# Kernel tuning notes

Hardware: AMD Instinct MI355X
Metric: run time of the kernel (lower is better)

Reference implementation:

```python
import jax, jax.numpy as jnp
import numpy as np

B, N, F, H, D, V = 1024, 64, 512, 512, 64, 16
NT = 6  # n_transform_params
SPLITS = [V * NT, NT, 1, V, V]
NOUT = sum(SPLITS)  # 135


def _make_transform(p):
    # p: [..., 6] -> similarity transform matrix [..., 3, 3], nonlinear=True
    sx, sy, theta, shear, tx, ty = [p[..., i] for i in range(6)]
    scale = jax.nn.sigmoid(sx) + 1e-2
    tx = jnp.tanh(tx * 5.0)
    ty = jnp.tanh(ty * 5.0)
    theta = theta * (2.0 * np.pi)
    c, s = jnp.cos(theta), jnp.sin(theta)
    zeros = jnp.zeros_like(scale)
    ones = jnp.ones_like(scale)
    row0 = jnp.stack([scale * c, -scale * s, tx], -1)
    row1 = jnp.stack([scale * s, scale * c, ty], -1)
    row2 = jnp.stack([zeros, zeros, ones], -1)
    return jnp.stack([row0, row1, row2], -2)


def setup_inputs() -> dict:
    key = jax.random.key(0)
    ks = jax.random.split(key, 12)
    feature = jax.random.normal(ks[0], (B, N, F), jnp.float32)
    # per-capsule feature MLP: F -> H -> D (with bias, ReLU between)
    mlp_w1 = jax.random.normal(ks[1], (N, F, H), jnp.float32) / np.sqrt(F)
    mlp_b1 = jnp.zeros((N, H), jnp.float32)
    mlp_w2 = jax.random.normal(ks[2], (N, H, D), jnp.float32) / np.sqrt(H)
    mlp_b2 = jnp.zeros((N, D), jnp.float32)
    # per-capsule caps MLP (bias=False): (D+1) -> H -> NOUT
    caps_w1 = jax.random.normal(ks[3], (N, D + 1, H), jnp.float32) / np.sqrt(D + 1)
    caps_w2 = jax.random.normal(ks[4], (N, H, NOUT), jnp.float32) / np.sqrt(H)
    # learned biases for outputs 1..4 and the static cpr
    bias_cvr = jnp.zeros((1, N, 1, NT), jnp.float32)
    bias_pl_caps = jnp.zeros((1, N, 1), jnp.float32)
    bias_pl_vote = jnp.zeros((1, N, V), jnp.float32)
    bias_scale = jnp.zeros((1, N, V), jnp.float32)
    cpr_static = jnp.zeros((1, N, V, NT), jnp.float32)
    return dict(feature=feature, mlp_w1=mlp_w1, mlp_b1=mlp_b1, mlp_w2=mlp_w2,
                mlp_b2=mlp_b2, caps_w1=caps_w1, caps_w2=caps_w2,
                bias_cvr=bias_cvr, bias_pl_caps=bias_pl_caps,
                bias_pl_vote=bias_pl_vote, bias_scale=bias_scale,
                cpr_static=cpr_static)


def reference(feature, mlp_w1, mlp_b1, mlp_w2, mlp_b2, caps_w1, caps_w2,
              bias_cvr, bias_pl_caps, bias_pl_vote, bias_scale, cpr_static):
    batch_size = feature.shape[0]
    # grouped per-capsule MLP over the capsule axis (replaces the python loop)
    h = jax.nn.relu(jnp.einsum('bnf,nfh->bnh', feature, mlp_w1) + mlp_b1[None])
    raw_caps_param = jnp.einsum('bnh,nhd->bnd', h, mlp_w2) + mlp_b2[None]  # [B,N,D]
    # dropout rate 0 -> caps_exist = ones
    caps_exist = jnp.ones((batch_size, N, 1), raw_caps_param.dtype)
    caps_param = jnp.concatenate([raw_caps_param, caps_exist], -1)  # [B,N,D+1]
    h2 = jax.nn.relu(jnp.einsum('bnd,ndh->bnh', caps_param, caps_w1))
    all_param = jnp.einsum('bnh,nho->bno', h2, caps_w2)  # [B,N,NOUT]
    offs = np.cumsum([0] + SPLITS)
    cpr_dynamic = all_param[..., offs[0]:offs[1]].reshape(batch_size, N, V, NT)
    cvr6 = all_param[..., offs[1]:offs[2]].reshape(batch_size, N, 1, NT)
    pl_caps = all_param[..., offs[2]:offs[3]].reshape(batch_size, N, 1)
    pl_vote = all_param[..., offs[3]:offs[4]].reshape(batch_size, N, V)
    scale6 = all_param[..., offs[4]:offs[5]].reshape(batch_size, N, V)
    cpr_dynamic_reg_loss = 0.5 * jnp.sum(cpr_dynamic ** 2) / batch_size
    cpr = _make_transform(cpr_dynamic + cpr_static)           # [B,N,V,3,3]
    cvr = _make_transform(cvr6 + bias_cvr)                     # [B,N,1,3,3]
    vote = jnp.matmul(cvr, cpr)                                # broadcast over V
    presence_logit_per_caps = pl_caps + bias_pl_caps
    presence_logit_per_vote = pl_vote + bias_pl_vote
    presence_per_vote = (jax.nn.sigmoid(presence_logit_per_caps)
                         * jax.nn.sigmoid(presence_logit_per_vote))
    # learn_vote_scale=True
    scale_per_vote = jax.nn.softplus(scale6 + bias_scale + 0.5) + 0.01
    return (vote, scale_per_vote, presence_per_vote,
            presence_logit_per_caps, presence_logit_per_vote,
            cpr_dynamic_reg_loss, raw_caps_param)
```

## Files before the change

kernel.cpp:

```cpp
#include <hip/hip_runtime.h>
#include <math.h>


#define BB    1024
#define NN    64
#define FF    512
#define HH    512
#define DD    64
#define VV    16
#define NTT   6
#define NOUTT 135

#define TBM     64
#define THREADS 512
#define NBLK    1024

typedef _Float16 f16;
typedef _Float16 f16x8 __attribute__((ext_vector_type(8)));
typedef float f32x4 __attribute__((ext_vector_type(4)));

#define MFMA16(a, b, c) __builtin_amdgcn_mfma_f32_16x16x32_f16((a), (b), (c), 0, 0, 0)
#define NTS(v, p)  __builtin_nontemporal_store((v), (p))

#define SZ_VOTE  ((size_t)BB*NN*VV*9)
#define OFF_VOTE  ((size_t)0)
#define OFF_SCALE (SZ_VOTE)
#define OFF_PRES  (OFF_SCALE + (size_t)BB*NN*VV)
#define OFF_PLC   (OFF_PRES  + (size_t)BB*NN*VV)
#define OFF_PLV   (OFF_PLC   + (size_t)BB*NN)
#define OFF_LOSS  (OFF_PLV   + (size_t)BB*NN*VV)
#define OFF_RAW   (OFF_LOSS  + 1)

#define WS_LOSSP 0
#define WS_W1H   ((size_t)8192)
#define WS_W2H   (WS_W1H  + 33554432)
#define WS_CW1H  (WS_W2H  + 4194304)
#define WS_CW2H  (WS_CW1H + 4194304)
#define WS_NEED  (WS_CW2H + 9437184)

__device__ __forceinline__ float sigmoidf_(float x) { return 1.f / (1.f + expf(-x)); }
__device__ __forceinline__ float softplusf_(float x) { return (x > 20.f) ? x : log1pf(expf(x)); }

__device__ __forceinline__ void make_tr(const float* p, float* M) {
  float scale = sigmoidf_(p[0]) + 1e-2f;
  float tx = tanhf(p[4] * 5.f);
  float ty = tanhf(p[5] * 5.f);
  float th = p[2] * 6.28318530717958647692f;
  float c = cosf(th), s = sinf(th);
  M[0] = scale * c; M[1] = -scale * s; M[2] = tx;
  M[3] = scale * s; M[4] =  scale * c; M[5] = ty;
  M[6] = 0.f;       M[7] = 0.f;        M[8] = 1.f;
}

__global__ void conv_fragB(const float* __restrict__ src, f16* __restrict__ dst,
                           int capStride, int Nsz, int Kc, int Nf) {
  const int tid = blockIdx.x * 256 + threadIdx.x;
  const int total = 64 * Kc * Nf * 64;
  if (tid >= total) return;
  const int c = tid & 15, g = (tid >> 4) & 3;
  int q = tid >> 6;
  const int nf = q % Nf; q /= Nf;
  const int kc = q % Kc; const int n = q / Kc;
  const int col = nf * 16 + c;
  const float* s = src + (size_t)n * capStride + (size_t)(kc * 32 + g * 8) * Nsz + col;
  f16x8 v;
  #pragma unroll
  for (int j = 0; j < 8; ++j) {
    float x = (col < Nsz) ? s[(size_t)j * Nsz] : 0.f;
    v[j] = (f16)x;
  }
  *(f16x8*)(dst + (size_t)tid * 8) = v;
}

__global__ __launch_bounds__(THREADS, 4)
void caps_mfma(const float* __restrict__ feature,
               const float* __restrict__ mlp_b1,
               const float* __restrict__ mlp_b2,
               const float* __restrict__ caps_w1,
               const f16*  __restrict__ w1h,
               const f16*  __restrict__ w2h,
               const f16*  __restrict__ cw1h,
               const f16*  __restrict__ cw2h,
               const float* __restrict__ bias_cvr,
               const float* __restrict__ bias_pl_caps,
               const float* __restrict__ bias_pl_vote,
               const float* __restrict__ bias_scale,
               const float* __restrict__ cpr_static,
               float* __restrict__ out,
               float* __restrict__ lossp)
{
  __shared__ __align__(16) f16 R0h[32768];
  __shared__ __align__(16) f16 Rraw[4096];
  __shared__ float red[8];

  const int t   = threadIdx.x;
  const int w   = t >> 6;
  const int ln  = t & 63;
  const int g   = ln >> 4;
  const int c16 = ln & 15;

  const int bid = blockIdx.x;
  const int xcd = bid & 7;
  const int j_  = bid >> 3;
  const int n   = (xcd << 3) + (j_ >> 4);
  const int b0  = (j_ & 15) * TBM;

  for (int rr = w; rr < 64; rr += 8) {
    const int mt = rr >> 4, kb = (rr & 15) * 4;
    const int koct = kb + g;
    const int brow = b0 + mt * 16 + c16;
    const float* fp = feature + ((size_t)brow * NN + n) * FF + koct * 8;
    const f32x4 f0 = __builtin_nontemporal_load((const f32x4*)fp);
    const f32x4 f1 = __builtin_nontemporal_load((const f32x4*)(fp + 4));
    f16x8 v;
    v[0]=(f16)f0.x; v[1]=(f16)f0.y; v[2]=(f16)f0.z; v[3]=(f16)f0.w;
    v[4]=(f16)f1.x; v[5]=(f16)f1.y; v[6]=(f16)f1.z; v[7]=(f16)f1.w;
    *(f16x8*)(R0h + mt * 8192 + koct * 128 + c16 * 8) = v;
  }
  __syncthreads();

  f32x4 acc[4][4];
  #pragma unroll
  for (int mt = 0; mt < 4; ++mt)
    #pragma unroll
    for (int nf = 0; nf < 4; ++nf) acc[mt][nf] = (f32x4)0.f;

  {
    const f16* wp = w1h + (size_t)n * 16 * 16384 + (size_t)(w * 4) * 512 + (size_t)ln * 8;
    f16x8 bA[4], bB[4];
    #pragma unroll
    for (int nf = 0; nf < 4; ++nf) bA[nf] = *(const f16x8*)(wp + (size_t)nf * 512);
    #pragma unroll
    for (int kc = 0; kc < 16; kc += 2) {
      #pragma unroll
      for (int nf = 0; nf < 4; ++nf)
        bB[nf] = *(const f16x8*)(wp + (size_t)(kc + 1) * 16384 + (size_t)nf * 512);
      f16x8 af[4];
      #pragma unroll
      for (int mt = 0; mt < 4; ++mt)
        af[mt] = *(const f16x8*)(R0h + mt * 8192 + (kc * 4 + g) * 128 + c16 * 8);
      #pragma unroll
      for (int nf = 0; nf < 4; ++nf)
        #pragma unroll
        for (int mt = 0; mt < 4; ++mt)
          acc[mt][nf] = MFMA16(af[mt], bA[nf], acc[mt][nf]);
      if (kc + 2 < 16) {
        #pragma unroll
        for (int nf = 0; nf < 4; ++nf)
          bA[nf] = *(const f16x8*)(wp + (size_t)(kc + 2) * 16384 + (size_t)nf * 512);
      }
      #pragma unroll
      for (int mt = 0; mt < 4; ++mt)
        af[mt] = *(const f16x8*)(R0h + mt * 8192 + ((kc + 1) * 4 + g) * 128 + c16 * 8);
      #pragma unroll
      for (int nf = 0; nf < 4; ++nf)
        #pragma unroll
        for (int mt = 0; mt < 4; ++mt)
          acc[mt][nf] = MFMA16(af[mt], bB[nf], acc[mt][nf]);
    }
  }
  __syncthreads();

  {
    const float* b1n = mlp_b1 + (size_t)n * HH;
    #pragma unroll
    for (int nf = 0; nf < 4; ++nf) {
      const int hcol = w * 64 + nf * 16 + c16;
      const float bb = b1n[hcol];
      const int koct = hcol >> 3, jj = hcol & 7;
      #pragma unroll
      for (int mt = 0; mt < 4; ++mt)
        #pragma unroll
        for (int r = 0; r < 4; ++r)
          R0h[mt * 8192 + koct * 128 + (g * 4 + r) * 8 + jj] =
              (f16)fmaxf(acc[mt][nf][r] + bb, 0.f);
    }
  }
  __syncthreads();

  {
    const int dnf = w & 3, mh = w >> 2;
    f32x4 accB0 = (f32x4)0.f, accB1 = (f32x4)0.f;
    const f16* w2p = w2h + (size_t)n * 16 * 2048 + (size_t)dnf * 512 + (size_t)ln * 8;
    f16x8 bw[16];
    #pragma unroll
    for (int kc = 0; kc < 16; ++kc) bw[kc] = *(const f16x8*)(w2p + (size_t)kc * 2048);
    #pragma unroll
    for (int kc = 0; kc < 16; ++kc) {
      const f16x8 af0 = *(const f16x8*)(R0h + (2 * mh)     * 8192 + (kc * 4 + g) * 128 + c16 * 8);
      const f16x8 af1 = *(const f16x8*)(R0h + (2 * mh + 1) * 8192 + (kc * 4 + g) * 128 + c16 * 8);
      accB0 = MFMA16(af0, bw[kc], accB0);
      accB1 = MFMA16(af1, bw[kc], accB1);
    }
    const int d = dnf * 16 + c16;
    const float bb2 = mlp_b2[(size_t)n * DD + d];
    const int koct = d >> 3, jj = d & 7;
    #pragma unroll
    for (int i = 0; i < 2; ++i) {
      const int mt = 2 * mh + i;
      const f32x4 a = i ? accB1 : accB0;
      #pragma unroll
      for (int r = 0; r < 4; ++r) {
        const int m = mt * 16 + g * 4 + r;
        const float v = a[r] + bb2;
        NTS(v, &out[OFF_RAW + (((size_t)(b0 + m)) * NN + n) * DD + d]);
        Rraw[mt * 1024 + koct * 128 + (g * 4 + r) * 8 + jj] = (f16)v;
      }
    }
  }
  __syncthreads();

  #pragma unroll
  for (int mt = 0; mt < 4; ++mt)
    #pragma unroll
    for (int nf = 0; nf < 4; ++nf) acc[mt][nf] = (f32x4)0.f;
  {
    const f16* cw1p = cw1h + (size_t)n * 2 * 16384 + (size_t)(w * 4) * 512 + (size_t)ln * 8;
    f16x8 bc0[4], bc1[4];
    #pragma unroll
    for (int nf = 0; nf < 4; ++nf) bc0[nf] = *(const f16x8*)(cw1p + (size_t)nf * 512);
    #pragma unroll
    for (int nf = 0; nf < 4; ++nf) bc1[nf] = *(const f16x8*)(cw1p + 16384 + (size_t)nf * 512);
    #pragma unroll
    for (int kc = 0; kc < 2; ++kc) {
      f16x8 af[4];
      #pragma unroll
      for (int mt = 0; mt < 4; ++mt)
        af[mt] = *(const f16x8*)(Rraw + mt * 1024 + (kc * 4 + g) * 128 + c16 * 8);
      #pragma unroll
      for (int nf = 0; nf < 4; ++nf)
        #pragma unroll
        for (int mt = 0; mt < 4; ++mt)
          acc[mt][nf] = MFMA16(af[mt], kc ? bc1[nf] : bc0[nf], acc[mt][nf]);
    }
    const float* cl = caps_w1 + ((size_t)n * 65 + 64) * HH;
    #pragma unroll
    for (int nf = 0; nf < 4; ++nf) {
      const int hcol = w * 64 + nf * 16 + c16;
      const float ev = cl[hcol];
      const int koct = hcol >> 3, jj = hcol & 7;
      #pragma unroll
      for (int mt = 0; mt < 4; ++mt)
        #pragma unroll
        for (int r = 0; r < 4; ++r)
          R0h[mt * 8192 + koct * 128 + (g * 4 + r) * 8 + jj] =
              (f16)fmaxf(acc[mt][nf][r] + ev, 0.f);
    }
  }
  __syncthreads();

  f32x4 accD[4];
  f32x4 accD8[4];
  #pragma unroll
  for (int mt = 0; mt < 4; ++mt) { accD[mt] = (f32x4)0.f; accD8[mt] = (f32x4)0.f; }
  {
    const f16* cw2p = cw2h + (size_t)n * 16 * 4608 + (size_t)ln * 8;
    const bool w0 = (w == 0);
    f16x8 dA, dB, dA8, dB8;
    dA = *(const f16x8*)(cw2p + (size_t)w * 512);
    if (w0) dA8 = *(const f16x8*)(cw2p + (size_t)8 * 512);
    #pragma unroll
    for (int kc = 0; kc < 16; kc += 2) {
      dB = *(const f16x8*)(cw2p + (size_t)(kc + 1) * 4608 + (size_t)w * 512);
      if (w0) dB8 = *(const f16x8*)(cw2p + (size_t)(kc + 1) * 4608 + (size_t)8 * 512);
      f16x8 af[4];
      #pragma unroll
      for (int mt = 0; mt < 4; ++mt)
        af[mt] = *(const f16x8*)(R0h + mt * 8192 + (kc * 4 + g) * 128 + c16 * 8);
      #pragma unroll
      for (int mt = 0; mt < 4; ++mt) accD[mt] = MFMA16(af[mt], dA, accD[mt]);
      if (w0) {
        #pragma unroll
        for (int mt = 0; mt < 4; ++mt) accD8[mt] = MFMA16(af[mt], dA8, accD8[mt]);
      }
      if (kc + 2 < 16) {
        dA = *(const f16x8*)(cw2p + (size_t)(kc + 2) * 4608 + (size_t)w * 512);
        if (w0) dA8 = *(const f16x8*)(cw2p + (size_t)(kc + 2) * 4608 + (size_t)8 * 512);
      }
      #pragma unroll
      for (int mt = 0; mt < 4; ++mt)
        af[mt] = *(const f16x8*)(R0h + mt * 8192 + ((kc + 1) * 4 + g) * 128 + c16 * 8);
      #pragma unroll
      for (int mt = 0; mt < 4; ++mt) accD[mt] = MFMA16(af[mt], dB, accD[mt]);
      if (w0) {
        #pragma unroll
        for (int mt = 0; mt < 4; ++mt) accD8[mt] = MFMA16(af[mt], dB8, accD8[mt]);
      }
    }
  }
  __syncthreads();

  float* apf = (float*)R0h;
  {
    const int col = w * 16 + c16;
    #pragma unroll
    for (int mt = 0; mt < 4; ++mt)
      #pragma unroll
      for (int r = 0; r < 4; ++r)
        apf[(size_t)(mt * 16 + g * 4 + r) * 145 + col] = accD[mt][r];
    if (w == 0) {
      const int col8 = 128 + c16;
      if (col8 < NOUTT) {
        #pragma unroll
        for (int mt = 0; mt < 4; ++mt)
          #pragma unroll
          for (int r = 0; r < 4; ++r)
            apf[(size_t)(mt * 16 + g * 4 + r) * 145 + col8] = accD8[mt][r];
      }
    }
  }
  __syncthreads();

  {
    const int mrow = t >> 3, seg = t & 7;
    const float* ar = apf + (size_t)mrow * 145 + seg * 12;
    float ls = 0.f;
    #pragma unroll
    for (int i = 0; i < 12; ++i) ls += ar[i] * ar[i];
    ls += __shfl_down(ls, 32); ls += __shfl_down(ls, 16); ls += __shfl_down(ls, 8);
    ls += __shfl_down(ls, 4);  ls += __shfl_down(ls, 2);  ls += __shfl_down(ls, 1);
    if (ln == 0) red[w] = ls;
    __syncthreads();
    if (t == 0) {
      float s = 0.f;
      #pragma unroll
      for (int i = 0; i < 8; ++i) s += red[i];
      lossp[bid] = s;
    }
  }

  for (int vt = t; vt < TBM * VV; vt += THREADS) {
    const int m = vt >> 4;
    const int v = vt & 15;
    const float* aprow = apf + (size_t)m * 145;
    float pd[6], pc[6];
    #pragma unroll
    for (int ii = 0; ii < 6; ++ii)
      pd[ii] = aprow[v * NTT + ii] + cpr_static[((size_t)n * VV + v) * NTT + ii];
    #pragma unroll
    for (int ii = 0; ii < 6; ++ii)
      pc[ii] = aprow[96 + ii] + bias_cvr[(size_t)n * NTT + ii];
    float Ma[9], Mb[9], Mv[9];
    make_tr(pc, Ma);
    make_tr(pd, Mb);
    #pragma unroll
    for (int r = 0; r < 3; ++r)
      #pragma unroll
      for (int c = 0; c < 3; ++c)
        Mv[r * 3 + c] = Ma[r*3+0] * Mb[0*3+c] + Ma[r*3+1] * Mb[1*3+c] + Ma[r*3+2] * Mb[2*3+c];
    const int b = b0 + m;
    const size_t vbase = (((size_t)b * NN + n) * VV + v) * 9;
    #pragma unroll
    for (int k = 0; k < 9; ++k) NTS(Mv[k], &out[OFF_VOTE + vbase + k]);
    const size_t sidx = ((size_t)b * NN + n) * VV + v;
    NTS(softplusf_(aprow[119 + v] + bias_scale[(size_t)n * VV + v] + 0.5f) + 0.01f,
        &out[OFF_SCALE + sidx]);
    const float plv = aprow[103 + v] + bias_pl_vote[(size_t)n * VV + v];
    NTS(plv, &out[OFF_PLV + sidx]);
    const float plc = aprow[102] + bias_pl_caps[n];
    if (v == 0) NTS(plc, &out[OFF_PLC + (size_t)b * NN + n]);
    NTS(sigmoidf_(plc) * sigmoidf_(plv), &out[OFF_PRES + sidx]);
  }
}

struct SA  { float featT[16][36]; float w1c[16][512]; };
struct SBp { float hbuf[32][128]; float w2c[128][64]; };
struct SC  { float cpT[64][32];  float cw1c[16][512]; };
struct SD  { float h2buf[32][68]; float cw2c[64][168]; };
struct SP  { float ap[32][136]; };
union  SH  { SA a; SBp b; SC c; SD d; SP p; };

__global__ __launch_bounds__(256)
void caps_fp32(const float* __restrict__ feature, const float* __restrict__ mlp_w1,
               const float* __restrict__ mlp_b1, const float* __restrict__ mlp_w2,
               const float* __restrict__ mlp_b2, const float* __restrict__ caps_w1,
               const float* __restrict__ caps_w2, const float* __restrict__ bias_cvr,
               const float* __restrict__ bias_pl_caps, const float* __restrict__ bias_pl_vote,
               const float* __restrict__ bias_scale, const float* __restrict__ cpr_static,
               float* __restrict__ out, float* __restrict__ lossp)
{
  __shared__ SH sh;
  __shared__ float red4[4];
  const int t  = threadIdx.x;
  const int wv = t >> 6;
  const int ln = t & 63;
  const int m0 = wv << 3;
  const int cA0 = ln << 2;
  const int cA1 = 256 + (ln << 2);
  const int bid   = blockIdx.x;
  const int xcd   = bid & 7;
  const int j     = bid >> 3;
  const int n     = (xcd << 3) + (j >> 5);
  const int mtile = j & 31;
  const int b0    = mtile * 32;

  float acc[64];
  #pragma unroll
  for (int i = 0; i < 64; ++i) acc[i] = 0.f;
  {
    const float* w1n = mlp_w1 + (size_t)n * FF * HH;
    for (int k0 = 0; k0 < FF; k0 += 16) {
      for (int e = t; e < 512; e += 256) {
        const int mm = e >> 4, kk = e & 15;
        sh.a.featT[kk][mm] = feature[(((size_t)(b0 + mm)) * NN + n) * FF + (k0 + kk)];
      }
      { const float4* src = (const float4*)(w1n + (size_t)k0 * HH);
        float4* dst = (float4*)sh.a.w1c;
        for (int u = t; u < 2048; u += 256) dst[u] = src[u]; }
      __syncthreads();
      #pragma unroll 4
      for (int kk = 0; kk < 16; ++kk) {
        const float4 a0  = *(const float4*)&sh.a.featT[kk][m0];
        const float4 a1  = *(const float4*)&sh.a.featT[kk][m0 + 4];
        const float4 bv0 = *(const float4*)&sh.a.w1c[kk][cA0];
        const float4 bv1 = *(const float4*)&sh.a.w1c[kk][cA1];
        const float av[8] = {a0.x, a0.y, a0.z, a0.w, a1.x, a1.y, a1.z, a1.w};
        const float bv[8] = {bv0.x, bv0.y, bv0.z, bv0.w, bv1.x, bv1.y, bv1.z, bv1.w};
        #pragma unroll
        for (int i = 0; i < 8; ++i)
          #pragma unroll
          for (int c = 0; c < 8; ++c) acc[i * 8 + c] += av[i] * bv[c];
      }
      __syncthreads();
    }
    const float* b1n = mlp_b1 + (size_t)n * HH;
    const float4 bb0 = *(const float4*)&b1n[cA0];
    const float4 bb1 = *(const float4*)&b1n[cA1];
    const float bb[8] = {bb0.x, bb0.y, bb0.z, bb0.w, bb1.x, bb1.y, bb1.z, bb1.w};
    #pragma unroll
    for (int i = 0; i < 8; ++i)
      #pragma unroll
      for (int c = 0; c < 8; ++c) acc[i * 8 + c] = fmaxf(acc[i * 8 + c] + bb[c], 0.f);
  }
  float rac[8];
  #pragma unroll
  for (int i = 0; i < 8; ++i) rac[i] = 0.f;
  {
    const float4* w2base = (const float4*)(mlp_w2 + (size_t)n * HH * DD);
    for (int q = 0; q < 4; ++q) {
      if (q == (ln >> 5)) {
        const int lc = (ln & 31) << 2;
        #pragma unroll
        for (int i = 0; i < 8; ++i)
          *(float4*)&sh.b.hbuf[m0 + i][lc] = make_float4(acc[i*8+0], acc[i*8+1], acc[i*8+2], acc[i*8+3]);
      }
      if (q == 2 + (ln >> 5)) {
        const int lc = (ln & 31) << 2;
        #pragma unroll
        for (int i = 0; i < 8; ++i)
          *(float4*)&sh.b.hbuf[m0 + i][lc] = make_float4(acc[i*8+4], acc[i*8+5], acc[i*8+6], acc[i*8+7]);
      }
      { const float4* src = w2base + (size_t)q * 2048;
        float4* dst = (float4*)sh.b.w2c;
        for (int u = t; u < 2048; u += 256) dst[u] = src[u]; }
      __syncthreads();
      #pragma unroll 2
      for (int kk = 0; kk < 128; kk += 4) {
        const float w0  = sh.b.w2c[kk + 0][ln];
        const float w1_ = sh.b.w2c[kk + 1][ln];
        const float w2_ = sh.b.w2c[kk + 2][ln];
        const float w3_ = sh.b.w2c[kk + 3][ln];
        #pragma unroll
        for (int i = 0; i < 8; ++i) {
          const float4 h4 = *(const float4*)&sh.b.hbuf[m0 + i][kk];
          rac[i] += h4.x * w0 + h4.y * w1_ + h4.z * w2_ + h4.w * w3_;
        }
      }
      __syncthreads();
    }
    const float bb2 = mlp_b2[(size_t)n * DD + ln];
    #pragma unroll
    for (int i = 0; i < 8; ++i) {
      const float rv = rac[i] + bb2;
      out[OFF_RAW + (((size_t)(b0 + m0 + i)) * NN + n) * DD + ln] = rv;
      sh.c.cpT[ln][(m0 + i + ln) & 31] = rv;
    }
  }
  #pragma unroll
  for (int i = 0; i < 64; ++i) acc[i] = 0.f;
  {
    const float* cw1n = caps_w1 + (size_t)n * (DD + 1) * HH;
    for (int k0 = 0; k0 < 64; k0 += 16) {
      const float4* src = (const float4*)(cw1n + (size_t)k0 * HH);
      float4* dst = (float4*)sh.c.cw1c;
      for (int u = t; u < 2048; u += 256) dst[u] = src[u];
      __syncthreads();
      #pragma unroll 4
      for (int kk = 0; kk < 16; ++kk) {
        const int k = k0 + kk;
        float av[8];
        #pragma unroll
        for (int i = 0; i < 8; ++i) av[i] = sh.c.cpT[k][(m0 + i + k) & 31];
        const float4 bv0 = *(const float4*)&sh.c.cw1c[kk][cA0];
        const float4 bv1 = *(const float4*)&sh.c.cw1c[kk][cA1];
        const float bv[8] = {bv0.x, bv0.y, bv0.z, bv0.w, bv1.x, bv1.y, bv1.z, bv1.w};
        #pragma unroll
        for (int i = 0; i < 8; ++i)
          #pragma unroll
          for (int c = 0; c < 8; ++c) acc[i * 8 + c] += av[i] * bv[c];
      }
      __syncthreads();
    }
    const float* cl = cw1n + (size_t)64 * HH;
    const float4 e0 = *(const float4*)&cl[cA0];
    const float4 e1 = *(const float4*)&cl[cA1];
    const float ev[8] = {e0.x, e0.y, e0.z, e0.w, e1.x, e1.y, e1.z, e1.w};
    #pragma unroll
    for (int i = 0; i < 8; ++i)
      #pragma unroll
      for (int c = 0; c < 8; ++c) acc[i * 8 + c] = fmaxf(acc[i * 8 + c] + ev[c], 0.f);
  }
  float ap[17];
  #pragma unroll
  for (int i = 0; i < 17; ++i) ap[i] = 0.f;
  const int mD = t >> 3;
  const int cD = t & 7;
  {
    const float* cw2n = caps_w2 + (size_t)n * HH * NOUTT;
    for (int q = 0; q < 8; ++q) {
      if (q == (ln >> 4)) {
        const int lc = (ln & 15) << 2;
        #pragma unroll
        for (int i = 0; i < 8; ++i)
          *(float4*)&sh.d.h2buf[m0 + i][lc] = make_float4(acc[i*8+0], acc[i*8+1], acc[i*8+2], acc[i*8+3]);
      }
      if (q == 4 + (ln >> 4)) {
        const int lc = (ln & 15) << 2;
        #pragma unroll
        for (int i = 0; i < 8; ++i)
          *(float4*)&sh.d.h2buf[m0 + i][lc] = make_float4(acc[i*8+4], acc[i*8+5], acc[i*8+6], acc[i*8+7]);
      }
      { const float* wsrc = cw2n + (size_t)(q << 6) * NOUTT;
        for (int r = wv; r < 64; r += 4)
          for (int c = ln; c < NOUTT; c += 64)
            sh.d.cw2c[r][c + ((c >> 4) << 2)] = wsrc[(size_t)r * NOUTT + c]; }
      __syncthreads();
      const int base20 = 20 * cD;
      #pragma unroll 2
      for (int kk = 0; kk < 64; ++kk) {
        const float hv = sh.d.h2buf[mD][kk];
        const float4 wa = *(const float4*)&sh.d.cw2c[kk][base20 + 0];
        const float4 wb = *(const float4*)&sh.d.cw2c[kk][base20 + 4];
        const float4 wc = *(const float4*)&sh.d.cw2c[kk][base20 + 8];
        const float4 wd = *(const float4*)&sh.d.cw2c[kk][base20 + 12];
        ap[0]  += hv * wa.x; ap[1]  += hv * wa.y; ap[2]  += hv * wa.z; ap[3]  += hv * wa.w;
        ap[4]  += hv * wb.x; ap[5]  += hv * wb.y; ap[6]  += hv * wb.z; ap[7]  += hv * wb.w;
        ap[8]  += hv * wc.x; ap[9]  += hv * wc.y; ap[10] += hv * wc.z; ap[11] += hv * wc.w;
        ap[12] += hv * wd.x; ap[13] += hv * wd.y; ap[14] += hv * wd.z; ap[15] += hv * wd.w;
        if (cD < 7) ap[16] += hv * sh.d.cw2c[kk][160 + cD];
      }
      __syncthreads();
    }
  }
  #pragma unroll
  for (int i = 0; i < 16; ++i) sh.p.ap[mD][(cD << 4) + i] = ap[i];
  if (cD < 7) sh.p.ap[mD][128 + cD] = ap[16];
  float ls = 0.f;
  if (cD < 6) {
    #pragma unroll
    for (int i = 0; i < 16; ++i) ls += ap[i] * ap[i];
  }
  __syncthreads();
  ls += __shfl_down(ls, 32); ls += __shfl_down(ls, 16); ls += __shfl_down(ls, 8);
  ls += __shfl_down(ls, 4);  ls += __shfl_down(ls, 2);  ls += __shfl_down(ls, 1);
  if (ln == 0) red4[wv] = ls;
  __syncthreads();
  if (t == 0) lossp[bid] = red4[0] + red4[1] + red4[2] + red4[3];
  for (int vt = t; vt < 32 * VV; vt += 256) {
    const int m = vt >> 4;
    const int v = vt & 15;
    const float* aprow = sh.p.ap[m];
    float pd[6], pc[6];
    #pragma unroll
    for (int ii = 0; ii < 6; ++ii)
      pd[ii] = aprow[v * NTT + ii] + cpr_static[((size_t)n * VV + v) * NTT + ii];
    #pragma unroll
    for (int ii = 0; ii < 6; ++ii)
      pc[ii] = aprow[96 + ii] + bias_cvr[(size_t)n * NTT + ii];
    float Ma[9], Mb[9], Mv[9];
    make_tr(pc, Ma);
    make_tr(pd, Mb);
    #pragma unroll
    for (int r = 0; r < 3; ++r)
      #pragma unroll
      for (int c = 0; c < 3; ++c)
        Mv[r * 3 + c] = Ma[r*3+0] * Mb[0*3+c] + Ma[r*3+1] * Mb[1*3+c] + Ma[r*3+2] * Mb[2*3+c];
    const int b = b0 + m;
    const size_t vbase = (((size_t)b * NN + n) * VV + v) * 9;
    #pragma unroll
    for (int k = 0; k < 9; ++k) out[OFF_VOTE + vbase + k] = Mv[k];
    const size_t sidx = ((size_t)b * NN + n) * VV + v;
    out[OFF_SCALE + sidx] = softplusf_(aprow[119 + v] + bias_scale[(size_t)n * VV + v] + 0.5f) + 0.01f;
    const float plv = aprow[103 + v] + bias_pl_vote[(size_t)n * VV + v];
    out[OFF_PLV + sidx] = plv;
    const float plc = aprow[102] + bias_pl_caps[n];
    if (v == 0) out[OFF_PLC + (size_t)b * NN + n] = plc;
    out[OFF_PRES + sidx] = sigmoidf_(plc) * sigmoidf_(plv);
  }
}

__global__ __launch_bounds__(256)
void loss_reduce(const float* __restrict__ lossp, float* __restrict__ out, int nblk) {
  __shared__ float r2[4];
  const int t = threadIdx.x;
  float s = 0.f;
  for (int i = t; i < nblk; i += 256) s += lossp[i];
  s += __shfl_down(s, 32); s += __shfl_down(s, 16); s += __shfl_down(s, 8);
  s += __shfl_down(s, 4);  s += __shfl_down(s, 2);  s += __shfl_down(s, 1);
  if ((t & 63) == 0) r2[t >> 6] = s;
  __syncthreads();
  if (t == 0) out[OFF_LOSS] = (r2[0] + r2[1] + r2[2] + r2[3]) * (0.5f / 1024.f);
}

extern "C" void kernel_launch(void* const* d_in, const int* in_sizes, int n_in,
                              void* d_out, int out_size, void* d_ws, size_t ws_size,
                              hipStream_t stream) {
  (void)in_sizes; (void)n_in; (void)out_size;
  const float* feature      = (const float*)d_in[0];
  const float* mlp_w1       = (const float*)d_in[1];
  const float* mlp_b1       = (const float*)d_in[2];
  const float* mlp_w2       = (const float*)d_in[3];
  const float* mlp_b2       = (const float*)d_in[4];
  const float* caps_w1      = (const float*)d_in[5];
  const float* caps_w2      = (const float*)d_in[6];
  const float* bias_cvr     = (const float*)d_in[7];
  const float* bias_pl_caps = (const float*)d_in[8];
  const float* bias_pl_vote = (const float*)d_in[9];
  const float* bias_scale   = (const float*)d_in[10];
  const float* cpr_static   = (const float*)d_in[11];
  float* out   = (float*)d_out;
  float* lossp = (float*)d_ws;

  if (ws_size >= WS_NEED) {
    f16* w1h  = (f16*)((char*)d_ws + WS_W1H);
    f16* w2h  = (f16*)((char*)d_ws + WS_W2H);
    f16* cw1h = (f16*)((char*)d_ws + WS_CW1H);
    f16* cw2h = (f16*)((char*)d_ws + WS_CW2H);
    hipLaunchKernelGGL(conv_fragB, dim3(2097152 / 256), dim3(256), 0, stream,
                       mlp_w1, w1h, 512 * 512, 512, 16, 32);
    hipLaunchKernelGGL(conv_fragB, dim3(262144 / 256), dim3(256), 0, stream,
                       mlp_w2, w2h, 512 * 64, 64, 16, 4);
    hipLaunchKernelGGL(conv_fragB, dim3(262144 / 256), dim3(256), 0, stream,
                       caps_w1, cw1h, 65 * 512, 512, 2, 32);
    hipLaunchKernelGGL(conv_fragB, dim3(589824 / 256), dim3(256), 0, stream,
                       caps_w2, cw2h, 512 * 135, 135, 16, 9);
    hipLaunchKernelGGL(caps_mfma, dim3(NBLK), dim3(THREADS), 0, stream,
                       feature, mlp_b1, mlp_b2, caps_w1, w1h, w2h, cw1h, cw2h,
                       bias_cvr, bias_pl_caps, bias_pl_vote, bias_scale, cpr_static,
                       out, lossp);
    hipLaunchKernelGGL(loss_reduce, dim3(1), dim3(256), 0, stream, lossp, out, NBLK);
  } else {
    hipLaunchKernelGGL(caps_fp32, dim3(2048), dim3(256), 0, stream,
                       feature, mlp_w1, mlp_b1, mlp_w2, mlp_b2, caps_w1, caps_w2,
                       bias_cvr, bias_pl_caps, bias_pl_vote, bias_scale, cpr_static,
                       out, lossp);
    hipLaunchKernelGGL(loss_reduce, dim3(1), dim3(256), 0, stream, lossp, out, 2048);
  }
}
```

Before: 145.3 us.

## Double the batch tile to 128 rows with 1024-thread blocks

Each block now handles 128 batch rows instead of 64, using 16 waves and half as many blocks. The first-layer K loop is split into two halves so the feature tile fits in one large shared buffer. Every weight fragment fetched from global memory is therefore reused across twice as many rows, which cuts per-block weight traffic. Each wave's work in every GEMM stage is redistributed to cover 8 row tiles and fewer column fragments. The cost is much higher LDS use per block (about 147KB), so only one block fits per CU, plus a tighter register budget under the launch bounds, which risks spills and lower latency hiding.

```diff
diff --git a/kernel.cpp b/kernel.cpp
--- a/kernel.cpp
+++ b/kernel.cpp
@@ -11,9 +11,9 @@
 #define NTT   6
 #define NOUTT 135
 
-#define TBM     64
-#define THREADS 512
-#define NBLK    1024
+#define TBM     128
+#define THREADS 1024
+#define NBLK    512
 
 typedef _Float16 f16;
 typedef _Float16 f16x8 __attribute__((ext_vector_type(8)));
@@ -89,9 +89,9 @@
                float* __restrict__ out,
                float* __restrict__ lossp)
 {
-  __shared__ __align__(16) f16 R0h[32768];
-  __shared__ __align__(16) f16 Rraw[4096];
-  __shared__ float red[8];
+  __shared__ __align__(16) f16 BIG[73728];
+  __shared__ float red[16];
+  f16* Rraw = BIG + 65536;
 
   const int t   = threadIdx.x;
   const int w   = t >> 6;
@@ -102,78 +102,75 @@
   const int bid = blockIdx.x;
   const int xcd = bid & 7;
   const int j_  = bid >> 3;
-  const int n   = (xcd << 3) + (j_ >> 4);
-  const int b0  = (j_ & 15) * TBM;
-
-  for (int rr = w; rr < 64; rr += 8) {
-    const int mt = rr >> 4, kb = (rr & 15) * 4;
-    const int koct = kb + g;
-    const int brow = b0 + mt * 16 + c16;
-    const float* fp = feature + ((size_t)brow * NN + n) * FF + koct * 8;
-    const f32x4 f0 = __builtin_nontemporal_load((const f32x4*)fp);
-    const f32x4 f1 = __builtin_nontemporal_load((const f32x4*)(fp + 4));
-    f16x8 v;
-    v[0]=(f16)f0.x; v[1]=(f16)f0.y; v[2]=(f16)f0.z; v[3]=(f16)f0.w;
-    v[4]=(f16)f1.x; v[5]=(f16)f1.y; v[6]=(f16)f1.z; v[7]=(f16)f1.w;
-    *(f16x8*)(R0h + mt * 8192 + koct * 128 + c16 * 8) = v;
-  }
-  __syncthreads();
-
-  f32x4 acc[4][4];
-  #pragma unroll
-  for (int mt = 0; mt < 4; ++mt)
-    #pragma unroll
-    for (int nf = 0; nf < 4; ++nf) acc[mt][nf] = (f32x4)0.f;
-
-  {
-    const f16* wp = w1h + (size_t)n * 16 * 16384 + (size_t)(w * 4) * 512 + (size_t)ln * 8;
-    f16x8 bA[4], bB[4];
-    #pragma unroll
-    for (int nf = 0; nf < 4; ++nf) bA[nf] = *(const f16x8*)(wp + (size_t)nf * 512);
-    #pragma unroll
-    for (int kc = 0; kc < 16; kc += 2) {
-      #pragma unroll
-      for (int nf = 0; nf < 4; ++nf)
-        bB[nf] = *(const f16x8*)(wp + (size_t)(kc + 1) * 16384 + (size_t)nf * 512);
-      f16x8 af[4];
-      #pragma unroll
-      for (int mt = 0; mt < 4; ++mt)
-        af[mt] = *(const f16x8*)(R0h + mt * 8192 + (kc * 4 + g) * 128 + c16 * 8);
-      #pragma unroll
-      for (int nf = 0; nf < 4; ++nf)
-        #pragma unroll
-        for (int mt = 0; mt < 4; ++mt)
-          acc[mt][nf] = MFMA16(af[mt], bA[nf], acc[mt][nf]);
-      if (kc + 2 < 16) {
-        #pragma unroll
-        for (int nf = 0; nf < 4; ++nf)
-          bA[nf] = *(const f16x8*)(wp + (size_t)(kc + 2) * 16384 + (size_t)nf * 512);
-      }
-      #pragma unroll
-      for (int mt = 0; mt < 4; ++mt)
-        af[mt] = *(const f16x8*)(R0h + mt * 8192 + ((kc + 1) * 4 + g) * 128 + c16 * 8);
-      #pragma unroll
-      for (int nf = 0; nf < 4; ++nf)
-        #pragma unroll
-        for (int mt = 0; mt < 4; ++mt)
-          acc[mt][nf] = MFMA16(af[mt], bB[nf], acc[mt][nf]);
-    }
-  }
-  __syncthreads();
+  const int n   = (xcd << 3) + (j_ >> 3);
+  const int b0  = (j_ & 7) * TBM;
+
+  f32x4 acc[8][2];
+  #pragma unroll
+  for (int mt = 0; mt < 8; ++mt) { acc[mt][0] = (f32x4)0.f; acc[mt][1] = (f32x4)0.f; }
+
+  for (int kh = 0; kh < 2; ++kh) {
+    for (int rr = w; rr < 64; rr += 16) {
+      const int mt = rr >> 3, kb = (rr & 7) * 4;
+      const int koctl = kb + g;
+      const int brow = b0 + mt * 16 + c16;
+      const float* fp = feature + ((size_t)brow * NN + n) * FF + (size_t)(kh * 32 + koctl) * 8;
+      const f32x4 f0 = __builtin_nontemporal_load((const f32x4*)fp);
+      const f32x4 f1 = __builtin_nontemporal_load((const f32x4*)(fp + 4));
+      f16x8 v;
+      v[0]=(f16)f0.x; v[1]=(f16)f0.y; v[2]=(f16)f0.z; v[3]=(f16)f0.w;
+      v[4]=(f16)f1.x; v[5]=(f16)f1.y; v[6]=(f16)f1.z; v[7]=(f16)f1.w;
+      *(f16x8*)(BIG + mt * 4096 + koctl * 128 + c16 * 8) = v;
+    }
+    __syncthreads();
+
+    const f16* wp = w1h + (size_t)n * 262144 + (size_t)(kh * 8) * 16384
+                  + (size_t)(2 * w) * 512 + (size_t)ln * 8;
+    f16x8 bA[2], bB[2];
+    bA[0] = *(const f16x8*)(wp);
+    bA[1] = *(const f16x8*)(wp + 512);
+    #pragma unroll
+    for (int kcl = 0; kcl < 8; kcl += 2) {
+      bB[0] = *(const f16x8*)(wp + (size_t)(kcl + 1) * 16384);
+      bB[1] = *(const f16x8*)(wp + (size_t)(kcl + 1) * 16384 + 512);
+      f16x8 af[8];
+      #pragma unroll
+      for (int mt = 0; mt < 8; ++mt)
+        af[mt] = *(const f16x8*)(BIG + mt * 4096 + (kcl * 4 + g) * 128 + c16 * 8);
+      #pragma unroll
+      for (int d = 0; d < 2; ++d)
+        #pragma unroll
+        for (int mt = 0; mt < 8; ++mt)
+          acc[mt][d] = MFMA16(af[mt], bA[d], acc[mt][d]);
+      if (kcl + 2 < 8) {
+        bA[0] = *(const f16x8*)(wp + (size_t)(kcl + 2) * 16384);
+        bA[1] = *(const f16x8*)(wp + (size_t)(kcl + 2) * 16384 + 512);
+      }
+      #pragma unroll
+      for (int mt = 0; mt < 8; ++mt)
+        af[mt] = *(const f16x8*)(BIG + mt * 4096 + ((kcl + 1) * 4 + g) * 128 + c16 * 8);
+      #pragma unroll
+      for (int d = 0; d < 2; ++d)
+        #pragma unroll
+        for (int mt = 0; mt < 8; ++mt)
+          acc[mt][d] = MFMA16(af[mt], bB[d], acc[mt][d]);
+    }
+    __syncthreads();
+  }
 
   {
     const float* b1n = mlp_b1 + (size_t)n * HH;
     #pragma unroll
-    for (int nf = 0; nf < 4; ++nf) {
-      const int hcol = w * 64 + nf * 16 + c16;
+    for (int d = 0; d < 2; ++d) {
+      const int hcol = w * 32 + d * 16 + c16;
       const float bb = b1n[hcol];
       const int koct = hcol >> 3, jj = hcol & 7;
       #pragma unroll
-      for (int mt = 0; mt < 4; ++mt)
+      for (int mt = 0; mt < 8; ++mt)
         #pragma unroll
         for (int r = 0; r < 4; ++r)
-          R0h[mt * 8192 + koct * 128 + (g * 4 + r) * 8 + jj] =
-              (f16)fmaxf(acc[mt][nf][r] + bb, 0.f);
+          BIG[mt * 8192 + koct * 128 + (g * 4 + r) * 8 + jj] =
+              (f16)fmaxf(acc[mt][d][r] + bb, 0.f);
     }
   }
   __syncthreads();
@@ -181,14 +178,14 @@
   {
     const int dnf = w & 3, mh = w >> 2;
     f32x4 accB0 = (f32x4)0.f, accB1 = (f32x4)0.f;
-    const f16* w2p = w2h + (size_t)n * 16 * 2048 + (size_t)dnf * 512 + (size_t)ln * 8;
+    const f16* w2p = w2h + (size_t)n * 32768 + (size_t)dnf * 512 + (size_t)ln * 8;
     f16x8 bw[16];
     #pragma unroll
     for (int kc = 0; kc < 16; ++kc) bw[kc] = *(const f16x8*)(w2p + (size_t)kc * 2048);
     #pragma unroll
     for (int kc = 0; kc < 16; ++kc) {
-      const f16x8 af0 = *(const f16x8*)(R0h + (2 * mh)     * 8192 + (kc * 4 + g) * 128 + c16 * 8);
-      const f16x8 af1 = *(const f16x8*)(R0h + (2 * mh + 1) * 8192 + (kc * 4 + g) * 128 + c16 * 8);
+      const f16x8 af0 = *(const f16x8*)(BIG + (2 * mh)     * 8192 + (kc * 4 + g) * 128 + c16 * 8);
+      const f16x8 af1 = *(const f16x8*)(BIG + (2 * mh + 1) * 8192 + (kc * 4 + g) * 128 + c16 * 8);
       accB0 = MFMA16(af0, bw[kc], accB0);
       accB1 = MFMA16(af1, bw[kc], accB1);
     }
@@ -211,101 +208,100 @@
   __syncthreads();
 
   #pragma unroll
-  for (int mt = 0; mt < 4; ++mt)
-    #pragma unroll
-    for (int nf = 0; nf < 4; ++nf) acc[mt][nf] = (f32x4)0.f;
-  {
-    const f16* cw1p = cw1h + (size_t)n * 2 * 16384 + (size_t)(w * 4) * 512 + (size_t)ln * 8;
-    f16x8 bc0[4], bc1[4];
-    #pragma unroll
-    for (int nf = 0; nf < 4; ++nf) bc0[nf] = *(const f16x8*)(cw1p + (size_t)nf * 512);
-    #pragma unroll
-    for (int nf = 0; nf < 4; ++nf) bc1[nf] = *(const f16x8*)(cw1p + 16384 + (size_t)nf * 512);
+  for (int mt = 0; mt < 8; ++mt) { acc[mt][0] = (f32x4)0.f; acc[mt][1] = (f32x4)0.f; }
+  {
+    const f16* cw1p = cw1h + (size_t)n * 32768 + (size_t)(2 * w) * 512 + (size_t)ln * 8;
+    f16x8 bc0[2], bc1[2];
+    bc0[0] = *(const f16x8*)(cw1p);
+    bc0[1] = *(const f16x8*)(cw1p + 512);
+    bc1[0] = *(const f16x8*)(cw1p + 16384);
+    bc1[1] = *(const f16x8*)(cw1p + 16384 + 512);
     #pragma unroll
     for (int kc = 0; kc < 2; ++kc) {
-      f16x8 af[4];
-      #pragma unroll
-      for (int mt = 0; mt < 4; ++mt)
+      f16x8 af[8];
+      #pragma unroll
+      for (int mt = 0; mt < 8; ++mt)
         af[mt] = *(const f16x8*)(Rraw + mt * 1024 + (kc * 4 + g) * 128 + c16 * 8);
       #pragma unroll
-      for (int nf = 0; nf < 4; ++nf)
-        #pragma unroll
-        for (int mt = 0; mt < 4; ++mt)
-          acc[mt][nf] = MFMA16(af[mt], kc ? bc1[nf] : bc0[nf], acc[mt][nf]);
+      for (int d = 0; d < 2; ++d)
+        #pragma unroll
+        for (int mt = 0; mt < 8; ++mt)
+          acc[mt][d] = MFMA16(af[mt], kc ? bc1[d] : bc0[d], acc[mt][d]);
     }
     const float* cl = caps_w1 + ((size_t)n * 65 + 64) * HH;
     #pragma unroll
-    for (int nf = 0; nf < 4; ++nf) {
-      const int hcol = w * 64 + nf * 16 + c16;
+    for (int d = 0; d < 2; ++d) {
+      const int hcol = w * 32 + d * 16 + c16;
       const float ev = cl[hcol];
       const int koct = hcol >> 3, jj = hcol & 7;
       #pragma unroll
-      for (int mt = 0; mt < 4; ++mt)
+      for (int mt = 0; mt < 8; ++mt)
         #pragma unroll
         for (int r = 0; r < 4; ++r)
-          R0h[mt * 8192 + koct * 128 + (g * 4 + r) * 8 + jj] =
-              (f16)fmaxf(acc[mt][nf][r] + ev, 0.f);
-    }
-  }
-  __syncthreads();
-
+          BIG[mt * 8192 + koct * 128 + (g * 4 + r) * 8 + jj] =
+              (f16)fmaxf(acc[mt][d][r] + ev, 0.f);
+    }
+  }
+  __syncthreads();
+
+  const int nfD = w & 7, mtb = (w >> 3) * 4;
+  const bool w8 = (w < 8);
+  const int mt8 = w;
   f32x4 accD[4];
-  f32x4 accD8[4];
-  #pragma unroll
-  for (int mt = 0; mt < 4; ++mt) { accD[mt] = (f32x4)0.f; accD8[mt] = (f32x4)0.f; }
-  {
-    const f16* cw2p = cw2h + (size_t)n * 16 * 4608 + (size_t)ln * 8;
-    const bool w0 = (w == 0);
+  f32x4 accD8;
+  #pragma unroll
+  for (int i = 0; i < 4; ++i) accD[i] = (f32x4)0.f;
+  accD8 = (f32x4)0.f;
+  {
+    const f16* cw2p = cw2h + (size_t)n * 73728 + (size_t)ln * 8;
     f16x8 dA, dB, dA8, dB8;
-    dA = *(const f16x8*)(cw2p + (size_t)w * 512);
-    if (w0) dA8 = *(const f16x8*)(cw2p + (size_t)8 * 512);
+    dA = *(const f16x8*)(cw2p + (size_t)nfD * 512);
+    if (w8) dA8 = *(const f16x8*)(cw2p + (size_t)8 * 512);
     #pragma unroll
     for (int kc = 0; kc < 16; kc += 2) {
-      dB = *(const f16x8*)(cw2p + (size_t)(kc + 1) * 4608 + (size_t)w * 512);
-      if (w0) dB8 = *(const f16x8*)(cw2p + (size_t)(kc + 1) * 4608 + (size_t)8 * 512);
+      dB = *(const f16x8*)(cw2p + (size_t)(kc + 1) * 4608 + (size_t)nfD * 512);
+      if (w8) dB8 = *(const f16x8*)(cw2p + (size_t)(kc + 1) * 4608 + (size_t)8 * 512);
       f16x8 af[4];
       #pragma unroll
-      for (int mt = 0; mt < 4; ++mt)
-        af[mt] = *(const f16x8*)(R0h + mt * 8192 + (kc * 4 + g) * 128 + c16 * 8);
-      #pragma unroll
-      for (int mt = 0; mt < 4; ++mt) accD[mt] = MFMA16(af[mt], dA, accD[mt]);
-      if (w0) {
-        #pragma unroll
-        for (int mt = 0; mt < 4; ++mt) accD8[mt] = MFMA16(af[mt], dA8, accD8[mt]);
+      for (int i = 0; i < 4; ++i)
+        af[i] = *(const f16x8*)(BIG + (mtb + i) * 8192 + (kc * 4 + g) * 128 + c16 * 8);
+      #pragma unroll
+      for (int i = 0; i < 4; ++i) accD[i] = MFMA16(af[i], dA, accD[i]);
+      if (w8) {
+        const f16x8 af8 = *(const f16x8*)(BIG + mt8 * 8192 + (kc * 4 + g) * 128 + c16 * 8);
+        accD8 = MFMA16(af8, dA8, accD8);
       }
       if (kc + 2 < 16) {
-        dA = *(const f16x8*)(cw2p + (size_t)(kc + 2) * 4608 + (size_t)w * 512);
-        if (w0) dA8 = *(const f16x8*)(cw2p + (size_t)(kc + 2) * 4608 + (size_t)8 * 512);
-      }
-      #pragma unroll
-      for (int mt = 0; mt < 4; ++mt)
-        af[mt] = *(const f16x8*)(R0h + mt * 8192 + ((kc + 1) * 4 + g) * 128 + c16 * 8);
-      #pragma unroll
-      for (int mt = 0; mt < 4; ++mt) accD[mt] = MFMA16(af[mt], dB, accD[mt]);
-      if (w0) {
-        #pragma unroll
-        for (int mt = 0; mt < 4; ++mt) accD8[mt] = MFMA16(af[mt], dB8, accD8[mt]);
-      }
-    }
-  }
-  __syncthreads();
-
-  float* apf = (float*)R0h;
-  {
-    const int col = w * 16 + c16;
-    #pragma unroll
-    for (int mt = 0; mt < 4; ++mt)
+        dA = *(const f16x8*)(cw2p + (size_t)(kc + 2) * 4608 + (size_t)nfD * 512);
+        if (w8) dA8 = *(const f16x8*)(cw2p + (size_t)(kc + 2) * 4608 + (size_t)8 * 512);
+      }
+      #pragma unroll
+      for (int i = 0; i < 4; ++i)
+        af[i] = *(const f16x8*)(BIG + (mtb + i) * 8192 + ((kc + 1) * 4 + g) * 128 + c16 * 8);
+      #pragma unroll
+      for (int i = 0; i < 4; ++i) accD[i] = MFMA16(af[i], dB, accD[i]);
+      if (w8) {
+        const f16x8 af8 = *(const f16x8*)(BIG + mt8 * 8192 + ((kc + 1) * 4 + g) * 128 + c16 * 8);
+        accD8 = MFMA16(af8, dB8, accD8);
+      }
+    }
+  }
+  __syncthreads();
+
+  float* apf = (float*)BIG;
+  {
+    const int col = nfD * 16 + c16;
+    #pragma unroll
+    for (int i = 0; i < 4; ++i)
       #pragma unroll
       for (int r = 0; r < 4; ++r)
-        apf[(size_t)(mt * 16 + g * 4 + r) * 145 + col] = accD[mt][r];
-    if (w == 0) {
+        apf[(size_t)((mtb + i) * 16 + g * 4 + r) * 145 + col] = accD[i][r];
+    if (w8) {
       const int col8 = 128 + c16;
       if (col8 < NOUTT) {
         #pragma unroll
-        for (int mt = 0; mt < 4; ++mt)
-          #pragma unroll
-          for (int r = 0; r < 4; ++r)
-            apf[(size_t)(mt * 16 + g * 4 + r) * 145 + col8] = accD8[mt][r];
+        for (int r = 0; r < 4; ++r)
+          apf[(size_t)(mt8 * 16 + g * 4 + r) * 145 + col8] = accD8[r];
       }
     }
   }
@@ -324,7 +320,7 @@
     if (t == 0) {
       float s = 0.f;
       #pragma unroll
-      for (int i = 0; i < 8; ++i) s += red[i];
+      for (int i = 0; i < 16; ++i) s += red[i];
       lossp[bid] = s;
     }
   }
```

Result: slower. 169.4 us (+16.6%).
